# Kernel tuning notes

Measured on AMD Instinct MI355X. Metric: run time of the kernel, lower is better.

Reference implementation:

```python
import jax, jax.numpy as jnp
import numpy as np

C = 512
NUM_HEADS = 8
NUM_GROUPS = 32
EPS = 1e-6


def group_norm(x, gamma, beta):
    # x: [B, C, N]
    b, c, n = x.shape
    xg = x.reshape(b, NUM_GROUPS, (c // NUM_GROUPS) * n)
    mean = xg.mean(axis=-1, keepdims=True)
    var = xg.var(axis=-1, keepdims=True)
    xg = (xg - mean) * jax.lax.rsqrt(var + EPS)
    x = xg.reshape(b, c, n)
    return x * gamma[None, :, None] + beta[None, :, None]


def conv1x1(x, w, bias):
    # pointwise conv: w [out_c, in_c], x [B, C, N]
    return jnp.einsum('oc,bcn->bon', w, x) + bias[None, :, None]


def setup_inputs() -> dict:
    key = jax.random.key(0)
    ks = jax.random.split(key, 11)
    s = 1.0 / np.sqrt(C)
    inp = {
        'x': jax.random.normal(ks[0], (4, C, 2048), dtype=jnp.float32),
        'gn_gamma': jnp.ones((C,), jnp.float32),
        'gn_beta': jnp.zeros((C,), jnp.float32),
        'q_w': jax.random.uniform(ks[1], (C, C), jnp.float32, -s, s),
        'q_b': jax.random.uniform(ks[2], (C,), jnp.float32, -s, s),
        'k_w': jax.random.uniform(ks[3], (C, C), jnp.float32, -s, s),
        'k_b': jax.random.uniform(ks[4], (C,), jnp.float32, -s, s),
        'v_w': jax.random.uniform(ks[5], (C, C), jnp.float32, -s, s),
        'v_b': jax.random.uniform(ks[6], (C,), jnp.float32, -s, s),
        'proj_w': jax.random.uniform(ks[7], (C, C), jnp.float32, -s, s),
        'proj_b': jax.random.uniform(ks[8], (C,), jnp.float32, -s, s),
    }
    return inp


def reference(x, gn_gamma, gn_beta, q_w, q_b, k_w, k_b, v_w, v_b, proj_w, proj_b):
    b, c, n = x.shape
    hc = c // NUM_HEADS
    h_ = group_norm(x, gn_gamma, gn_beta)
    q = conv1x1(h_, q_w, q_b)
    k = conv1x1(h_, k_w, k_b)
    v = conv1x1(h_, v_w, v_b)
    # split heads: [B, H, hc, N]
    q = q.reshape(b, NUM_HEADS, hc, n)
    k = k.reshape(b, NUM_HEADS, hc, n)
    v = v.reshape(b, NUM_HEADS, hc, n)
    # NOTE: scale uses full channel count c, matching the original code
    scale = jnp.asarray(c, x.dtype) ** -0.5
    # scores: [B, H, Nq, Nk]
    w = jnp.einsum('bhcn,bhcm->bhnm', q, k) * scale
    w = jax.nn.softmax(w, axis=-1)
    # out[b,h,c,q] = sum_m v[b,h,c,m] * w[b,h,q,m]
    out = jnp.einsum('bhcm,bhqm->bhcq', v, w)
    out = out.reshape(b, c, n)
    out = conv1x1(out, proj_w, proj_b)
    return x + out
```

## Files before the change

kernel.cpp:

```cpp
#include <hip/hip_runtime.h>
#include <hip/hip_bf16.h>
#include <math.h>

#define C_DIM 512
#define N_DIM 2048
#define B_DIM 4
#define NGRP 32
#define GCH 16
#define NHEAD 8
#define HDIM 64
#define EPSV 1e-6f

using f32x4  = __attribute__((ext_vector_type(4))) float;
using bf16x8 = __attribute__((ext_vector_type(8))) short;

#define GLL16(gp, lp) __builtin_amdgcn_global_load_lds( \
    (const __attribute__((address_space(1))) unsigned int*)(gp), \
    (__attribute__((address_space(3))) unsigned int*)(lp), 16, 0, 0)

#define BFPACK(a, b) __builtin_amdgcn_perm(__float_as_uint(b), __float_as_uint(a), 0x07060302u)

static __device__ __forceinline__ unsigned short f2bf(float f) {
    union { __hip_bfloat16 h; unsigned short u; } cv;
    cv.h = __float2bfloat16(f);
    return cv.u;
}

__global__ __launch_bounds__(256) void gn_stats(const float* __restrict__ x,
                                                float* __restrict__ partial) {
    const int HSZ = GCH * N_DIM / 2;
    int blk = blockIdx.x;
    const float4* x4 = (const float4*)(x + (size_t)blk * HSZ);
    int tid = threadIdx.x;

    float s = 0.f, ss = 0.f;
    #pragma unroll
    for (int it = 0; it < HSZ / 4 / 256; ++it) {
        float4 v = x4[tid + it * 256];
        s  += v.x + v.y + v.z + v.w;
        ss += v.x * v.x + v.y * v.y + v.z * v.z + v.w * v.w;
    }
    __shared__ float rs[256], rss[256];
    rs[tid] = s; rss[tid] = ss;
    __syncthreads();
    for (int off = 128; off > 0; off >>= 1) {
        if (tid < off) { rs[tid] += rs[tid + off]; rss[tid] += rss[tid + off]; }
        __syncthreads();
    }
    if (tid == 0) {
        partial[blk * 2]     = rs[0];
        partial[blk * 2 + 1] = rss[0];
    }
}

__global__ __launch_bounds__(256) void gn_apply_t(const float* __restrict__ x,
                                                  const float* __restrict__ partial,
                                                  const float* __restrict__ gamma,
                                                  const float* __restrict__ beta,
                                                  unsigned short* __restrict__ ht) {
    __shared__ char smem[8192];
    const float GSZI = 1.f / (GCH * N_DIM);
    int n0 = blockIdx.x * 64, c0 = blockIdx.y * 64, b = blockIdx.z;
    int tid = threadIdx.x;
    #pragma unroll
    for (int it = 0; it < 4; ++it) {
        int idx = tid + it * 256;
        int ci = idx >> 4, n4 = (idx & 15) << 2;
        int cg = c0 + ci, grp = cg >> 4;
        int bg = b * NGRP + grp;
        float s  = partial[bg * 4]     + partial[bg * 4 + 2];
        float ss = partial[bg * 4 + 1] + partial[bg * 4 + 3];
        float mean = s * GSZI;
        float var  = ss * GSZI - mean * mean;
        float rstd = rsqrtf(var + EPSV);
        float ga = gamma[cg] * rstd, be = beta[cg] - mean * ga;
        float4 v = *(const float4*)&x[((size_t)b * C_DIM + cg) * N_DIM + n0 + n4];
        float vals[4] = {v.x, v.y, v.z, v.w};
        #pragma unroll
        for (int j = 0; j < 4; ++j) {
            int nl = n4 + j;
            *(unsigned short*)(smem + nl * 128 + ((ci * 2) ^ ((nl & 7) << 4))) =
                f2bf(vals[j] * ga + be);
        }
    }
    __syncthreads();
    #pragma unroll
    for (int i = 0; i < 2; ++i) {
        int idx = tid + i * 256;
        int row = idx >> 3, ch = idx & 7;
        bf16x8 v = *(const bf16x8*)(smem + row * 128 + ((ch * 16) ^ ((row & 7) << 4)));
        *(bf16x8*)&ht[((size_t)(b * N_DIM + n0 + row)) * C_DIM + c0 + ch * 8] = v;
    }
}

__global__ __launch_bounds__(256) void cast4_bf16(const float* __restrict__ s0,
                                                  const float* __restrict__ s1,
                                                  const float* __restrict__ s2,
                                                  const float* __restrict__ s3,
                                                  unsigned short* __restrict__ dst) {
    int which = blockIdx.y;
    const float* src = (which == 0) ? s0 : (which == 1) ? s1 : (which == 2) ? s2 : s3;
    size_t idx = (size_t)blockIdx.x * 256 + threadIdx.x;
    const float4* s4 = (const float4*)src;
    float4 a = s4[idx * 2], b = s4[idx * 2 + 1];
    bf16x8 o;
    o[0] = (short)f2bf(a.x); o[1] = (short)f2bf(a.y);
    o[2] = (short)f2bf(a.z); o[3] = (short)f2bf(a.w);
    o[4] = (short)f2bf(b.x); o[5] = (short)f2bf(b.y);
    o[6] = (short)f2bf(b.z); o[7] = (short)f2bf(b.w);
    *(bf16x8*)&dst[(size_t)which * 262144 + idx * 8] = o;
}

__global__ __launch_bounds__(512) void conv_qkv(const unsigned short* __restrict__ Wall,
                                                const float* __restrict__ q_b,
                                                const float* __restrict__ k_b,
                                                const float* __restrict__ v_b,
                                                const unsigned short* __restrict__ ht,
                                                unsigned short* __restrict__ qt,
                                                unsigned short* __restrict__ kt,
                                                unsigned short* __restrict__ vt,
                                                float escale) {
    __shared__ char smem[40960];

    int bn0 = blockIdx.x * 128;
    int bo  = blockIdx.y * 64;
    int tid = threadIdx.x;
    int L = tid & 63, w = tid >> 6;
    int g = L >> 4, c = L & 15;
    int wr = w >> 2, wc = w & 3;

    f32x4 acc[3][2][2];
    #pragma unroll
    for (int w3 = 0; w3 < 3; ++w3)
        #pragma unroll
        for (int t = 0; t < 2; ++t)
            #pragma unroll
            for (int u = 0; u < 2; ++u) acc[w3][t][u] = f32x4{0.f, 0.f, 0.f, 0.f};

    for (int k0 = 0; k0 < C_DIM; k0 += 64) {
        if (w < 4) {
            #pragma unroll
            for (int i = 0; i < 4; ++i) {
                int j = w * 4 + i;
                int row = j * 8 + (L >> 3);
                int sl = (L & 7) ^ (row & 7);
                GLL16(ht + (size_t)(bn0 + row) * C_DIM + k0 + sl * 8, smem + j * 1024);
            }
        } else {
            #pragma unroll
            for (int i = 0; i < 6; ++i) {
                int j = (w - 4) * 6 + i;
                int w3 = j >> 3, jj = j & 7;
                int row = jj * 8 + (L >> 3);
                int sl = (L & 7) ^ (row & 7);
                GLL16(Wall + (size_t)w3 * 262144 + (size_t)(bo + row) * C_DIM + k0 + sl * 8,
                      smem + 16384 + j * 1024);
            }
        }
        __syncthreads();

        bf16x8 bfr[2][2];
        #pragma unroll
        for (int u = 0; u < 2; ++u) {
            int row = wc * 32 + u * 16 + c;
            #pragma unroll
            for (int ks = 0; ks < 2; ++ks)
                bfr[u][ks] = *(const bf16x8*)(smem + row * 128 +
                                              ((g * 16 + ks * 64) ^ ((row & 7) << 4)));
        }
        #pragma unroll
        for (int w3 = 0; w3 < 3; ++w3) {
            char* As = smem + 16384 + w3 * 8192;
            bf16x8 af[2][2];
            #pragma unroll
            for (int t = 0; t < 2; ++t) {
                int row = wr * 32 + t * 16 + c;
                #pragma unroll
                for (int ks = 0; ks < 2; ++ks)
                    af[t][ks] = *(const bf16x8*)(As + row * 128 +
                                                 ((g * 16 + ks * 64) ^ ((row & 7) << 4)));
            }
            #pragma unroll
            for (int ks = 0; ks < 2; ++ks)
                #pragma unroll
                for (int t = 0; t < 2; ++t)
                    #pragma unroll
                    for (int u = 0; u < 2; ++u)
                        acc[w3][t][u] = __builtin_amdgcn_mfma_f32_16x16x32_bf16(
                            af[t][ks], bfr[u][ks], acc[w3][t][u], 0, 0, 0);
        }
        __syncthreads();
    }

    int b  = bn0 >> 11;
    int nb = bn0 & (N_DIM - 1);
    int hh = bo >> 6;
    int bh = b * NHEAD + hh;

    #pragma unroll
    for (int t = 0; t < 2; ++t)
        #pragma unroll
        for (int r = 0; r < 4; ++r) {
            int m = bo + wr * 32 + t * 16 + g * 4 + r;
            float bi = v_b[m];
            #pragma unroll
            for (int u = 0; u < 2; ++u) {
                int n = nb + wc * 32 + u * 16 + c;
                vt[((size_t)b * C_DIM + m) * N_DIM + n] = f2bf(acc[2][t][u][r] + bi);
            }
        }

    char* Ts = smem;
    #pragma unroll
    for (int pass = 0; pass < 2; ++pass) {
        const float* bias = pass ? k_b : q_b;
        float esc = pass ? 1.0f : escale;
        unsigned short* dst = pass ? kt : qt;
        __syncthreads();
        #pragma unroll
        for (int t = 0; t < 2; ++t)
            #pragma unroll
            for (int r = 0; r < 4; ++r) {
                int ml = wr * 32 + t * 16 + g * 4 + r;
                float bi = bias[bo + ml];
                #pragma unroll
                for (int u = 0; u < 2; ++u) {
                    int nl = wc * 32 + u * 16 + c;
                    *(unsigned short*)(Ts + nl * 128 + ((ml * 2) ^ ((nl & 7) << 4))) =
                        f2bf((acc[pass][t][u][r] + bi) * esc);
                }
            }
        __syncthreads();
        #pragma unroll
        for (int i = 0; i < 2; ++i) {
            int idx = tid + i * 512;
            int row = idx >> 3, ch = idx & 7;
            bf16x8 v = *(const bf16x8*)(Ts + row * 128 + ((ch * 16) ^ ((row & 7) << 4)));
            *(bf16x8*)&dst[((size_t)bh * N_DIM + nb + row) * HDIM + ch * 8] = v;
        }
    }
}

__global__ __launch_bounds__(256) void conv_proj(const unsigned short* __restrict__ Wb,
                                                 const float* __restrict__ bias,
                                                 const unsigned short* __restrict__ Bsrc,
                                                 const float* __restrict__ res,
                                                 float* __restrict__ outf) {
    __shared__ char smem[24576];
    int bn0 = blockIdx.x * 128;
    int bo  = blockIdx.y * 64;
    int tid = threadIdx.x;
    int L = tid & 63, w = tid >> 6;
    int g = L >> 4, c = L & 15;
    int wr = w >> 1, wc = w & 1;

    f32x4 acc[2][4];
    #pragma unroll
    for (int t = 0; t < 2; ++t)
        #pragma unroll
        for (int u = 0; u < 4; ++u) acc[t][u] = f32x4{0.f, 0.f, 0.f, 0.f};

    for (int k0 = 0; k0 < C_DIM; k0 += 64) {
        #pragma unroll
        for (int i = 0; i < 2; ++i) {
            int j = w * 2 + i;
            int ra = j * 8 + (L >> 3);
            int sl = (L & 7) ^ (ra & 7);
            GLL16(Wb + (size_t)(bo + ra) * C_DIM + k0 + sl * 8, smem + j * 1024);
        }
        #pragma unroll
        for (int i = 0; i < 4; ++i) {
            int j = w * 4 + i;
            int rb = j * 8 + (L >> 3);
            int sl = (L & 7) ^ (rb & 7);
            GLL16(Bsrc + (size_t)(bn0 + rb) * C_DIM + k0 + sl * 8, smem + 8192 + j * 1024);
        }
        __syncthreads();

        bf16x8 af[2][2], bfr[4][2];
        #pragma unroll
        for (int t = 0; t < 2; ++t) {
            int row = wr * 32 + t * 16 + c;
            #pragma unroll
            for (int ks = 0; ks < 2; ++ks)
                af[t][ks] = *(const bf16x8*)(smem + row * 128 +
                                             ((g * 16 + ks * 64) ^ ((row & 7) << 4)));
        }
        #pragma unroll
        for (int u = 0; u < 4; ++u) {
            int row = wc * 64 + u * 16 + c;
            #pragma unroll
            for (int ks = 0; ks < 2; ++ks)
                bfr[u][ks] = *(const bf16x8*)(smem + 8192 + row * 128 +
                                              ((g * 16 + ks * 64) ^ ((row & 7) << 4)));
        }
        #pragma unroll
        for (int ks = 0; ks < 2; ++ks)
            #pragma unroll
            for (int t = 0; t < 2; ++t)
                #pragma unroll
                for (int u = 0; u < 4; ++u)
                    acc[t][u] = __builtin_amdgcn_mfma_f32_16x16x32_bf16(
                        af[t][ks], bfr[u][ks], acc[t][u], 0, 0, 0);
        __syncthreads();
    }

    int b  = bn0 >> 11;
    int nb = bn0 & (N_DIM - 1);
    #pragma unroll
    for (int t = 0; t < 2; ++t)
        #pragma unroll
        for (int r = 0; r < 4; ++r) {
            int m = bo + wr * 32 + t * 16 + g * 4 + r;
            float bi = bias[m];
            #pragma unroll
            for (int u = 0; u < 4; ++u) {
                int n = nb + wc * 64 + u * 16 + c;
                size_t off = ((size_t)b * C_DIM + m) * N_DIM + n;
                outf[off] = acc[t][u][r] + bi + res[off];
            }
        }
}

__global__ __launch_bounds__(512, 4) void attn_kernel(const unsigned short* __restrict__ Qt,
                                                      const unsigned short* __restrict__ Kt,
                                                      const unsigned short* __restrict__ Vt,
                                                      unsigned short* __restrict__ at) {
    __shared__ char smem[49152];

    int d = blockIdx.x;
    int xcd = d & 7;
    int slot = d >> 3;
    int bh = xcd + 8 * (slot >> 4);
    int q0 = (slot & 15) * 128;

    int b = bh >> 3, hh = bh & 7;
    int tid = threadIdx.x;
    int L = tid & 63, w = tid >> 6;
    int g = L >> 4, c = L & 15;

    const unsigned short* Qh = Qt + (size_t)bh * N_DIM * HDIM;
    const unsigned short* Kh = Kt + (size_t)bh * N_DIM * HDIM;
    const unsigned short* Vh = Vt + (size_t)bh * HDIM * N_DIM;

    #pragma unroll
    for (int i = 0; i < 2; ++i) {
        int j = w * 2 + i;
        int row = j * 8 + (L >> 3);
        int sl = (L & 7) ^ (row & 7);
        GLL16(Qh + (size_t)(q0 + row) * HDIM + sl * 8, smem + j * 1024);
    }
    int srow = w * 8 + (L >> 3);
    int ssl  = (L & 7) ^ (srow & 7);
    GLL16(Kh + (size_t)srow * HDIM + ssl * 8, smem + 16384 + w * 1024);
    GLL16(Vh + (size_t)srow * N_DIM + ssl * 8, smem + 24576 + w * 1024);
    __syncthreads();

    int csw = (c & 7) << 4;
    char* kb0 = smem + 16384 + c * 128 + ((g * 16) ^ csw);
    char* kb1 = smem + 16384 + c * 128 + ((g * 16 + 64) ^ csw);
    char* pb  = smem + (w * 16 + c) * 128;
    char* pw0 = pb + ((g * 8) ^ csw);
    char* pw1 = pb + ((32 + g * 8) ^ csw);
    char* pw2 = pb + ((64 + g * 8) ^ csw);
    char* pw3 = pb + ((96 + g * 8) ^ csw);
    char* pr0 = pb + ((g * 16) ^ csw);
    char* pr1 = pb + ((64 + g * 16) ^ csw);

    bf16x8 qf[2];
    qf[0] = *(const bf16x8*)pr0;
    qf[1] = *(const bf16x8*)pr1;

    const unsigned short* kgp = Kh + (size_t)(64 + srow) * HDIM + ssl * 8;
    const unsigned short* vgp = Vh + (size_t)srow * N_DIM + 64 + ssl * 8;

    f32x4 oacc[4];
    #pragma unroll
    for (int t = 0; t < 4; ++t) oacc[t] = f32x4{0.f, 0.f, 0.f, 0.f};
    float m_r = -INFINITY, l_part = 0.f;

    auto tile = [&](int BOFF) {
        f32x4 sacc[4];
        #pragma unroll
        for (int t = 0; t < 4; ++t) sacc[t] = f32x4{0.f, 0.f, 0.f, 0.f};
        __builtin_amdgcn_s_setprio(1);
        #pragma unroll
        for (int t = 0; t < 4; ++t) {
            bf16x8 kf0 = *(const bf16x8*)(kb0 + BOFF + t * 2048);
            bf16x8 kf1 = *(const bf16x8*)(kb1 + BOFF + t * 2048);
            sacc[t] = __builtin_amdgcn_mfma_f32_16x16x32_bf16(kf0, qf[0], sacc[t], 0, 0, 0);
            sacc[t] = __builtin_amdgcn_mfma_f32_16x16x32_bf16(kf1, qf[1], sacc[t], 0, 0, 0);
        }
        __builtin_amdgcn_s_setprio(0);

        float t0 = fmaxf(fmaxf(sacc[0][0], sacc[0][1]), sacc[0][2]);
        float t1 = fmaxf(fmaxf(sacc[0][3], sacc[1][0]), sacc[1][1]);
        float t2 = fmaxf(fmaxf(sacc[1][2], sacc[1][3]), sacc[2][0]);
        float t3 = fmaxf(fmaxf(sacc[2][1], sacc[2][2]), sacc[2][3]);
        float t4 = fmaxf(fmaxf(sacc[3][0], sacc[3][1]), sacc[3][2]);
        float mloc = fmaxf(fmaxf(fmaxf(t0, t1), fmaxf(t2, t3)), fmaxf(t4, sacc[3][3]));
        if (!__all(mloc - m_r <= 6.0f)) {
            mloc = fmaxf(mloc, __shfl_xor(mloc, 16));
            mloc = fmaxf(mloc, __shfl_xor(mloc, 32));
            float mn = fmaxf(m_r, mloc);
            float fac = exp2f(m_r - mn);
            m_r = mn;
            l_part *= fac;
            #pragma unroll
            for (int t = 0; t < 4; ++t) oacc[t] = oacc[t] * fac;
        }
        f32x4 m4 = {m_r, m_r, m_r, m_r};
        f32x4 p[4];
        #pragma unroll
        for (int t = 0; t < 4; ++t) {
            f32x4 dd = sacc[t] - m4;
            p[t][0] = exp2f(dd[0]);
            p[t][1] = exp2f(dd[1]);
            p[t][2] = exp2f(dd[2]);
            p[t][3] = exp2f(dd[3]);
        }
        f32x4 racc = (p[0] + p[1]) + (p[2] + p[3]);
        l_part += (racc[0] + racc[1]) + (racc[2] + racc[3]);

        unsigned pk[4][2];
        #pragma unroll
        for (int t = 0; t < 4; ++t) {
            pk[t][0] = BFPACK(p[t][0], p[t][1]);
            pk[t][1] = BFPACK(p[t][2], p[t][3]);
        }

        *(unsigned long long*)pw0 = (unsigned long long)pk[0][0] | ((unsigned long long)pk[0][1] << 32);
        *(unsigned long long*)pw1 = (unsigned long long)pk[1][0] | ((unsigned long long)pk[1][1] << 32);
        *(unsigned long long*)pw2 = (unsigned long long)pk[2][0] | ((unsigned long long)pk[2][1] << 32);
        *(unsigned long long*)pw3 = (unsigned long long)pk[3][0] | ((unsigned long long)pk[3][1] << 32);

        __builtin_amdgcn_s_setprio(1);
        {
            bf16x8 pf0 = *(const bf16x8*)pr0;
            #pragma unroll
            for (int t = 0; t < 4; ++t) {
                bf16x8 vf = *(const bf16x8*)(kb0 + BOFF + 8192 + t * 2048);
                oacc[t] = __builtin_amdgcn_mfma_f32_16x16x32_bf16(vf, pf0, oacc[t], 0, 0, 0);
            }
            bf16x8 pf1 = *(const bf16x8*)pr1;
            #pragma unroll
            for (int t = 0; t < 4; ++t) {
                bf16x8 vf = *(const bf16x8*)(kb1 + BOFF + 8192 + t * 2048);
                oacc[t] = __builtin_amdgcn_mfma_f32_16x16x32_bf16(vf, pf1, oacc[t], 0, 0, 0);
            }
        }
        __builtin_amdgcn_s_setprio(0);
    };

    #define ATTN_BARRIER() do { \
        __builtin_amdgcn_s_barrier(); \
        asm volatile("" ::: "memory"); \
    } while (0)
    #define ATTN_VMCNT2() do { \
        asm volatile("s_waitcnt vmcnt(2)" ::: "memory"); \
        __builtin_amdgcn_sched_barrier(0); \
    } while (0)
    #define ATTN_VMCNT0() do { \
        asm volatile("s_waitcnt vmcnt(0)" ::: "memory"); \
        __builtin_amdgcn_sched_barrier(0); \
    } while (0)

    for (int i = 0; i < 15; ++i) {
        ATTN_BARRIER();
        GLL16(kgp, smem + 32768 + w * 1024);
        GLL16(vgp, smem + 40960 + w * 1024);
        kgp += 64 * HDIM;
        vgp += 64;
        ATTN_VMCNT2();
        tile(0);
        ATTN_BARRIER();
        GLL16(kgp, smem + 16384 + w * 1024);
        GLL16(vgp, smem + 24576 + w * 1024);
        kgp += 64 * HDIM;
        vgp += 64;
        ATTN_VMCNT2();
        tile(16384);
    }
    ATTN_BARRIER();
    GLL16(kgp, smem + 32768 + w * 1024);
    GLL16(vgp, smem + 40960 + w * 1024);
    ATTN_VMCNT2();
    tile(0);
    ATTN_BARRIER();
    ATTN_VMCNT0();
    tile(16384);

    #undef ATTN_BARRIER
    #undef ATTN_VMCNT2
    #undef ATTN_VMCNT0

    float l_r = l_part;
    l_r += __shfl_xor(l_r, 16);
    l_r += __shfl_xor(l_r, 32);
    float oinv = 1.f / l_r;
    {
        unsigned lo, hi;
        lo = BFPACK(oacc[0][0] * oinv, oacc[0][1] * oinv);
        hi = BFPACK(oacc[0][2] * oinv, oacc[0][3] * oinv);
        *(unsigned long long*)pw0 = (unsigned long long)lo | ((unsigned long long)hi << 32);
        lo = BFPACK(oacc[1][0] * oinv, oacc[1][1] * oinv);
        hi = BFPACK(oacc[1][2] * oinv, oacc[1][3] * oinv);
        *(unsigned long long*)pw1 = (unsigned long long)lo | ((unsigned long long)hi << 32);
        lo = BFPACK(oacc[2][0] * oinv, oacc[2][1] * oinv);
        hi = BFPACK(oacc[2][2] * oinv, oacc[2][3] * oinv);
        *(unsigned long long*)pw2 = (unsigned long long)lo | ((unsigned long long)hi << 32);
        lo = BFPACK(oacc[3][0] * oinv, oacc[3][1] * oinv);
        hi = BFPACK(oacc[3][2] * oinv, oacc[3][3] * oinv);
        *(unsigned long long*)pw3 = (unsigned long long)lo | ((unsigned long long)hi << 32);
    }
    char* wbase = smem + w * 2048;
    #pragma unroll
    for (int i = 0; i < 2; ++i) {
        int idx = L + i * 64;
        int row = idx >> 3, ch = idx & 7;
        bf16x8 v = *(const bf16x8*)(wbase + row * 128 + ((ch * 16) ^ ((row & 7) << 4)));
        *(bf16x8*)&at[((size_t)(b * N_DIM + q0 + w * 16 + row)) * C_DIM + hh * HDIM + ch * 8] = v;
    }
}

extern "C" void kernel_launch(void* const* d_in, const int* in_sizes, int n_in,
                              void* d_out, int out_size, void* d_ws, size_t ws_size,
                              hipStream_t stream) {
    (void)in_sizes; (void)n_in; (void)out_size; (void)ws_size;
    const float* x     = (const float*)d_in[0];
    const float* gam   = (const float*)d_in[1];
    const float* bet   = (const float*)d_in[2];
    const float* q_w   = (const float*)d_in[3];
    const float* q_b   = (const float*)d_in[4];
    const float* k_w   = (const float*)d_in[5];
    const float* k_b   = (const float*)d_in[6];
    const float* v_w   = (const float*)d_in[7];
    const float* v_b   = (const float*)d_in[8];
    const float* p_w   = (const float*)d_in[9];
    const float* p_b   = (const float*)d_in[10];
    float* out = (float*)d_out;

    const size_t MB = 1 << 20;
    char* wsb = (char*)d_ws;
    unsigned short* ht  = (unsigned short*)(wsb);
    unsigned short* wqb = (unsigned short*)(wsb + 8 * MB);
    unsigned short* wpb = (unsigned short*)(wsb + 9 * MB + 512 * 1024);
    float*          partial = (float*)(wsb + 10 * MB);
    unsigned short* qt  = (unsigned short*)(wsb + 11 * MB);
    unsigned short* kt  = (unsigned short*)(wsb + 19 * MB);
    unsigned short* vt  = (unsigned short*)(wsb + 27 * MB);
    unsigned short* at  = (unsigned short*)(wsb + 35 * MB);

    gn_stats<<<B_DIM * NGRP * 2, 256, 0, stream>>>(x, partial);
    gn_apply_t<<<dim3(N_DIM / 64, C_DIM / 64, B_DIM), 256, 0, stream>>>(x, partial, gam, bet, ht);

    cast4_bf16<<<dim3(128, 4), 256, 0, stream>>>(q_w, k_w, v_w, p_w, wqb);

    const float escale = 0.044194173824159216f * 1.4426950408889634f;
    conv_qkv<<<dim3(B_DIM * N_DIM / 128, C_DIM / 64), 512, 0, stream>>>(
        wqb, q_b, k_b, v_b, ht, qt, kt, vt, escale);

    attn_kernel<<<512, 512, 0, stream>>>(qt, kt, vt, at);

    conv_proj<<<dim3(B_DIM * N_DIM / 128, C_DIM / 64), 256, 0, stream>>>(wpb, p_b, at, x, out);
}
```

Before: 113.4 us.

## Process two query sub-tiles per wave in attention to reuse K/V fragments

The attention kernel moves from 8 waves with 16 query rows each to 4 waves with 32 query rows each, held as two sub-tiles sharing every K and V fragment read from LDS. This halves LDS reads of K/V per query row and gives each wave more independent MFMAs to interleave. Each thread now issues twice as many async loads per stage, so the waitcnt changes from vmcnt(2) to vmcnt(4). The cost is higher register pressure and fewer waves per block to hide latency, with launch bounds moving from (512,4) to (256,2).

```diff
diff --git a/kernel.cpp b/kernel.cpp
--- a/kernel.cpp
+++ b/kernel.cpp
@@ -322,7 +322,7 @@
         }
 }
 
-__global__ __launch_bounds__(512, 4) void attn_kernel(const unsigned short* __restrict__ Qt,
+__global__ __launch_bounds__(256, 2) void attn_kernel(const unsigned short* __restrict__ Qt,
                                                       const unsigned short* __restrict__ Kt,
                                                       const unsigned short* __restrict__ Vt,
                                                       unsigned short* __restrict__ at) {
@@ -343,110 +343,134 @@
     const unsigned short* Kh = Kt + (size_t)bh * N_DIM * HDIM;
     const unsigned short* Vh = Vt + (size_t)bh * HDIM * N_DIM;
 
-    #pragma unroll
-    for (int i = 0; i < 2; ++i) {
-        int j = w * 2 + i;
+    int ssl = (L & 7) ^ (L >> 3);
+    #pragma unroll
+    for (int i = 0; i < 4; ++i) {
+        int j = w * 4 + i;
         int row = j * 8 + (L >> 3);
-        int sl = (L & 7) ^ (row & 7);
-        GLL16(Qh + (size_t)(q0 + row) * HDIM + sl * 8, smem + j * 1024);
-    }
-    int srow = w * 8 + (L >> 3);
-    int ssl  = (L & 7) ^ (srow & 7);
-    GLL16(Kh + (size_t)srow * HDIM + ssl * 8, smem + 16384 + w * 1024);
-    GLL16(Vh + (size_t)srow * N_DIM + ssl * 8, smem + 24576 + w * 1024);
+        GLL16(Qh + (size_t)(q0 + row) * HDIM + ssl * 8, smem + j * 1024);
+    }
+    int srow = w * 16 + (L >> 3);
+    GLL16(Kh + (size_t)srow * HDIM + ssl * 8,        smem + 16384 + (2 * w) * 1024);
+    GLL16(Kh + (size_t)(srow + 8) * HDIM + ssl * 8,  smem + 16384 + (2 * w + 1) * 1024);
+    GLL16(Vh + (size_t)srow * N_DIM + ssl * 8,       smem + 24576 + (2 * w) * 1024);
+    GLL16(Vh + (size_t)(srow + 8) * N_DIM + ssl * 8, smem + 24576 + (2 * w + 1) * 1024);
     __syncthreads();
 
     int csw = (c & 7) << 4;
     char* kb0 = smem + 16384 + c * 128 + ((g * 16) ^ csw);
     char* kb1 = smem + 16384 + c * 128 + ((g * 16 + 64) ^ csw);
-    char* pb  = smem + (w * 16 + c) * 128;
-    char* pw0 = pb + ((g * 8) ^ csw);
-    char* pw1 = pb + ((32 + g * 8) ^ csw);
-    char* pw2 = pb + ((64 + g * 8) ^ csw);
-    char* pw3 = pb + ((96 + g * 8) ^ csw);
-    char* pr0 = pb + ((g * 16) ^ csw);
-    char* pr1 = pb + ((64 + g * 16) ^ csw);
-
-    bf16x8 qf[2];
-    qf[0] = *(const bf16x8*)pr0;
-    qf[1] = *(const bf16x8*)pr1;
+    char* pb  = smem + (w * 32 + c) * 128;
+    int pwo0 = (g * 8) ^ csw;
+    int pwo1 = (32 + g * 8) ^ csw;
+    int pwo2 = (64 + g * 8) ^ csw;
+    int pwo3 = (96 + g * 8) ^ csw;
+    int pro0 = (g * 16) ^ csw;
+    int pro1 = (64 + g * 16) ^ csw;
+
+    bf16x8 qf[2][2];
+    #pragma unroll
+    for (int s = 0; s < 2; ++s) {
+        qf[s][0] = *(const bf16x8*)(pb + s * 2048 + pro0);
+        qf[s][1] = *(const bf16x8*)(pb + s * 2048 + pro1);
+    }
 
     const unsigned short* kgp = Kh + (size_t)(64 + srow) * HDIM + ssl * 8;
     const unsigned short* vgp = Vh + (size_t)srow * N_DIM + 64 + ssl * 8;
 
-    f32x4 oacc[4];
-    #pragma unroll
-    for (int t = 0; t < 4; ++t) oacc[t] = f32x4{0.f, 0.f, 0.f, 0.f};
-    float m_r = -INFINITY, l_part = 0.f;
+    f32x4 oacc[2][4];
+    #pragma unroll
+    for (int s = 0; s < 2; ++s)
+        #pragma unroll
+        for (int t = 0; t < 4; ++t) oacc[s][t] = f32x4{0.f, 0.f, 0.f, 0.f};
+    float m_r[2] = {-INFINITY, -INFINITY};
+    float l_part[2] = {0.f, 0.f};
 
     auto tile = [&](int BOFF) {
-        f32x4 sacc[4];
-        #pragma unroll
-        for (int t = 0; t < 4; ++t) sacc[t] = f32x4{0.f, 0.f, 0.f, 0.f};
+        f32x4 sacc[2][4];
+        #pragma unroll
+        for (int s = 0; s < 2; ++s)
+            #pragma unroll
+            for (int t = 0; t < 4; ++t) sacc[s][t] = f32x4{0.f, 0.f, 0.f, 0.f};
         __builtin_amdgcn_s_setprio(1);
         #pragma unroll
         for (int t = 0; t < 4; ++t) {
             bf16x8 kf0 = *(const bf16x8*)(kb0 + BOFF + t * 2048);
             bf16x8 kf1 = *(const bf16x8*)(kb1 + BOFF + t * 2048);
-            sacc[t] = __builtin_amdgcn_mfma_f32_16x16x32_bf16(kf0, qf[0], sacc[t], 0, 0, 0);
-            sacc[t] = __builtin_amdgcn_mfma_f32_16x16x32_bf16(kf1, qf[1], sacc[t], 0, 0, 0);
+            sacc[0][t] = __builtin_amdgcn_mfma_f32_16x16x32_bf16(kf0, qf[0][0], sacc[0][t], 0, 0, 0);
+            sacc[0][t] = __builtin_amdgcn_mfma_f32_16x16x32_bf16(kf1, qf[0][1], sacc[0][t], 0, 0, 0);
+            sacc[1][t] = __builtin_amdgcn_mfma_f32_16x16x32_bf16(kf0, qf[1][0], sacc[1][t], 0, 0, 0);
+            sacc[1][t] = __builtin_amdgcn_mfma_f32_16x16x32_bf16(kf1, qf[1][1], sacc[1][t], 0, 0, 0);
         }
         __builtin_amdgcn_s_setprio(0);
 
-        float t0 = fmaxf(fmaxf(sacc[0][0], sacc[0][1]), sacc[0][2]);
-        float t1 = fmaxf(fmaxf(sacc[0][3], sacc[1][0]), sacc[1][1]);
-        float t2 = fmaxf(fmaxf(sacc[1][2], sacc[1][3]), sacc[2][0]);
-        float t3 = fmaxf(fmaxf(sacc[2][1], sacc[2][2]), sacc[2][3]);
-        float t4 = fmaxf(fmaxf(sacc[3][0], sacc[3][1]), sacc[3][2]);
-        float mloc = fmaxf(fmaxf(fmaxf(t0, t1), fmaxf(t2, t3)), fmaxf(t4, sacc[3][3]));
-        if (!__all(mloc - m_r <= 6.0f)) {
-            mloc = fmaxf(mloc, __shfl_xor(mloc, 16));
-            mloc = fmaxf(mloc, __shfl_xor(mloc, 32));
-            float mn = fmaxf(m_r, mloc);
-            float fac = exp2f(m_r - mn);
-            m_r = mn;
-            l_part *= fac;
-            #pragma unroll
-            for (int t = 0; t < 4; ++t) oacc[t] = oacc[t] * fac;
-        }
-        f32x4 m4 = {m_r, m_r, m_r, m_r};
-        f32x4 p[4];
-        #pragma unroll
-        for (int t = 0; t < 4; ++t) {
-            f32x4 dd = sacc[t] - m4;
-            p[t][0] = exp2f(dd[0]);
-            p[t][1] = exp2f(dd[1]);
-            p[t][2] = exp2f(dd[2]);
-            p[t][3] = exp2f(dd[3]);
-        }
-        f32x4 racc = (p[0] + p[1]) + (p[2] + p[3]);
-        l_part += (racc[0] + racc[1]) + (racc[2] + racc[3]);
-
-        unsigned pk[4][2];
-        #pragma unroll
-        for (int t = 0; t < 4; ++t) {
-            pk[t][0] = BFPACK(p[t][0], p[t][1]);
-            pk[t][1] = BFPACK(p[t][2], p[t][3]);
-        }
-
-        *(unsigned long long*)pw0 = (unsigned long long)pk[0][0] | ((unsigned long long)pk[0][1] << 32);
-        *(unsigned long long*)pw1 = (unsigned long long)pk[1][0] | ((unsigned long long)pk[1][1] << 32);
-        *(unsigned long long*)pw2 = (unsigned long long)pk[2][0] | ((unsigned long long)pk[2][1] << 32);
-        *(unsigned long long*)pw3 = (unsigned long long)pk[3][0] | ((unsigned long long)pk[3][1] << 32);
+        float mloc[2];
+        #pragma unroll
+        for (int s = 0; s < 2; ++s) {
+            float t0 = fmaxf(fmaxf(sacc[s][0][0], sacc[s][0][1]), sacc[s][0][2]);
+            float t1 = fmaxf(fmaxf(sacc[s][0][3], sacc[s][1][0]), sacc[s][1][1]);
+            float t2 = fmaxf(fmaxf(sacc[s][1][2], sacc[s][1][3]), sacc[s][2][0]);
+            float t3 = fmaxf(fmaxf(sacc[s][2][1], sacc[s][2][2]), sacc[s][2][3]);
+            float t4 = fmaxf(fmaxf(sacc[s][3][0], sacc[s][3][1]), sacc[s][3][2]);
+            mloc[s] = fmaxf(fmaxf(fmaxf(t0, t1), fmaxf(t2, t3)), fmaxf(t4, sacc[s][3][3]));
+        }
+        float growth = fmaxf(mloc[0] - m_r[0], mloc[1] - m_r[1]);
+        if (!__all(growth <= 6.0f)) {
+            #pragma unroll
+            for (int s = 0; s < 2; ++s) {
+                float ms = mloc[s];
+                ms = fmaxf(ms, __shfl_xor(ms, 16));
+                ms = fmaxf(ms, __shfl_xor(ms, 32));
+                float mn = fmaxf(m_r[s], ms);
+                float fac = exp2f(m_r[s] - mn);
+                m_r[s] = mn;
+                l_part[s] *= fac;
+                #pragma unroll
+                for (int t = 0; t < 4; ++t) oacc[s][t] = oacc[s][t] * fac;
+            }
+        }
+        unsigned pk[2][4][2];
+        #pragma unroll
+        for (int s = 0; s < 2; ++s) {
+            f32x4 m4 = {m_r[s], m_r[s], m_r[s], m_r[s]};
+            f32x4 p[4];
+            #pragma unroll
+            for (int t = 0; t < 4; ++t) {
+                f32x4 dd = sacc[s][t] - m4;
+                p[t][0] = exp2f(dd[0]);
+                p[t][1] = exp2f(dd[1]);
+                p[t][2] = exp2f(dd[2]);
+                p[t][3] = exp2f(dd[3]);
+            }
+            f32x4 racc = (p[0] + p[1]) + (p[2] + p[3]);
+            l_part[s] += (racc[0] + racc[1]) + (racc[2] + racc[3]);
+            #pragma unroll
+            for (int t = 0; t < 4; ++t) {
+                pk[s][t][0] = BFPACK(p[t][0], p[t][1]);
+                pk[s][t][1] = BFPACK(p[t][2], p[t][3]);
+            }
+        }
+
+        #pragma unroll
+        for (int s = 0; s < 2; ++s) {
+            char* sb = pb + s * 2048;
+            *(unsigned long long*)(sb + pwo0) = (unsigned long long)pk[s][0][0] | ((unsigned long long)pk[s][0][1] << 32);
+            *(unsigned long long*)(sb + pwo1) = (unsigned long long)pk[s][1][0] | ((unsigned long long)pk[s][1][1] << 32);
+            *(unsigned long long*)(sb + pwo2) = (unsigned long long)pk[s][2][0] | ((unsigned long long)pk[s][2][1] << 32);
+            *(unsigned long long*)(sb + pwo3) = (unsigned long long)pk[s][3][0] | ((unsigned long long)pk[s][3][1] << 32);
+        }
 
         __builtin_amdgcn_s_setprio(1);
-        {
-            bf16x8 pf0 = *(const bf16x8*)pr0;
+        #pragma unroll
+        for (int ks = 0; ks < 2; ++ks) {
+            char* kbase = (ks == 0 ? kb0 : kb1) + BOFF + 8192;
+            bf16x8 pf0 = *(const bf16x8*)(pb + (ks ? pro1 : pro0));
+            bf16x8 pf1 = *(const bf16x8*)(pb + 2048 + (ks ? pro1 : pro0));
             #pragma unroll
             for (int t = 0; t < 4; ++t) {
-                bf16x8 vf = *(const bf16x8*)(kb0 + BOFF + 8192 + t * 2048);
-                oacc[t] = __builtin_amdgcn_mfma_f32_16x16x32_bf16(vf, pf0, oacc[t], 0, 0, 0);
-            }
-            bf16x8 pf1 = *(const bf16x8*)pr1;
-            #pragma unroll
-            for (int t = 0; t < 4; ++t) {
-                bf16x8 vf = *(const bf16x8*)(kb1 + BOFF + 8192 + t * 2048);
-                oacc[t] = __builtin_amdgcn_mfma_f32_16x16x32_bf16(vf, pf1, oacc[t], 0, 0, 0);
+                bf16x8 vf = *(const bf16x8*)(kbase + t * 2048);
+                oacc[0][t] = __builtin_amdgcn_mfma_f32_16x16x32_bf16(vf, pf0, oacc[0][t], 0, 0, 0);
+                oacc[1][t] = __builtin_amdgcn_mfma_f32_16x16x32_bf16(vf, pf1, oacc[1][t], 0, 0, 0);
             }
         }
         __builtin_amdgcn_s_setprio(0);
@@ -456,8 +480,8 @@
         __builtin_amdgcn_s_barrier(); \
         asm volatile("" ::: "memory"); \
     } while (0)
-    #define ATTN_VMCNT2() do { \
-        asm volatile("s_waitcnt vmcnt(2)" ::: "memory"); \
+    #define ATTN_VMCNT4() do { \
+        asm volatile("s_waitcnt vmcnt(4)" ::: "memory"); \
         __builtin_amdgcn_sched_barrier(0); \
     } while (0)
     #define ATTN_VMCNT0() do { \
@@ -467,59 +491,67 @@
 
     for (int i = 0; i < 15; ++i) {
         ATTN_BARRIER();
-        GLL16(kgp, smem + 32768 + w * 1024);
-        GLL16(vgp, smem + 40960 + w * 1024);
+        GLL16(kgp,              smem + 32768 + (2 * w) * 1024);
+        GLL16(kgp + 8 * HDIM,   smem + 32768 + (2 * w + 1) * 1024);
+        GLL16(vgp,              smem + 40960 + (2 * w) * 1024);
+        GLL16(vgp + 8 * N_DIM,  smem + 40960 + (2 * w + 1) * 1024);
         kgp += 64 * HDIM;
         vgp += 64;
-        ATTN_VMCNT2();
+        ATTN_VMCNT4();
         tile(0);
         ATTN_BARRIER();
-        GLL16(kgp, smem + 16384 + w * 1024);
-        GLL16(vgp, smem + 24576 + w * 1024);
+        GLL16(kgp,              smem + 16384 + (2 * w) * 1024);
+        GLL16(kgp + 8 * HDIM,   smem + 16384 + (2 * w + 1) * 1024);
+        GLL16(vgp,              smem + 24576 + (2 * w) * 1024);
+        GLL16(vgp + 8 * N_DIM,  smem + 24576 + (2 * w + 1) * 1024);
         kgp += 64 * HDIM;
         vgp += 64;
-        ATTN_VMCNT2();
+        ATTN_VMCNT4();
         tile(16384);
     }
     ATTN_BARRIER();
-    GLL16(kgp, smem + 32768 + w * 1024);
-    GLL16(vgp, smem + 40960 + w * 1024);
-    ATTN_VMCNT2();
+    GLL16(kgp,              smem + 32768 + (2 * w) * 1024);
+    GLL16(kgp + 8 * HDIM,   smem + 32768 + (2 * w + 1) * 1024);
+    GLL16(vgp,              smem + 40960 + (2 * w) * 1024);
+    GLL16(vgp + 8 * N_DIM,  smem + 40960 + (2 * w + 1) * 1024);
+    ATTN_VMCNT4();
     tile(0);
     ATTN_BARRIER();
     ATTN_VMCNT0();
     tile(16384);
 
     #undef ATTN_BARRIER
-    #undef ATTN_VMCNT2
+    #undef ATTN_VMCNT4
     #undef ATTN_VMCNT0
 
-    float l_r = l_part;
-    l_r += __shfl_xor(l_r, 16);
-    l_r += __shfl_xor(l_r, 32);
-    float oinv = 1.f / l_r;
-    {
+    #pragma unroll
+    for (int s = 0; s < 2; ++s) {
+        float l_r = l_part[s];
+        l_r += __shfl_xor(l_r, 16);
+        l_r += __shfl_xor(l_r, 32);
+        float oinv = 1.f / l_r;
+        char* sb = pb + s * 2048;
         unsigned lo, hi;
-        lo = BFPACK(oacc[0][0] * oinv, oacc[0][1] * oinv);
-        hi = BFPACK(oacc[0][2] * oinv, oacc[0][3] * oinv);
-        *(unsigned long long*)pw0 = (unsigned long long)lo | ((unsigned long long)hi << 32);
-        lo = BFPACK(oacc[1][0] * oinv, oacc[1][1] * oinv);
-        hi = BFPACK(oacc[1][2] * oinv, oacc[1][3] * oinv);
-        *(unsigned long long*)pw1 = (unsigned long long)lo | ((unsigned long long)hi << 32);
-        lo = BFPACK(oacc[2][0] * oinv, oacc[2][1] * oinv);
-        hi = BFPACK(oacc[2][2] * oinv, oacc[2][3] * oinv);
-        *(unsigned long long*)pw2 = (unsigned long long)lo | ((unsigned long long)hi << 32);
-        lo = BFPACK(oacc[3][0] * oinv, oacc[3][1] * oinv);
-        hi = BFPACK(oacc[3][2] * oinv, oacc[3][3] * oinv);
-        *(unsigned long long*)pw3 = (unsigned long long)lo | ((unsigned long long)hi << 32);
-    }
-    char* wbase = smem + w * 2048;
-    #pragma unroll
-    for (int i = 0; i < 2; ++i) {
+        lo = BFPACK(oacc[s][0][0] * oinv, oacc[s][0][1] * oinv);
+        hi = BFPACK(oacc[s][0][2] * oinv, oacc[s][0][3] * oinv);
+        *(unsigned long long*)(sb + pwo0) = (unsigned long long)lo | ((unsigned long long)hi << 32);
+        lo = BFPACK(oacc[s][1][0] * oinv, oacc[s][1][1] * oinv);
+        hi = BFPACK(oacc[s][1][2] * oinv, oacc[s][1][3] * oinv);
+        *(unsigned long long*)(sb + pwo1) = (unsigned long long)lo | ((unsigned long long)hi << 32);
+        lo = BFPACK(oacc[s][2][0] * oinv, oacc[s][2][1] * oinv);
+        hi = BFPACK(oacc[s][2][2] * oinv, oacc[s][2][3] * oinv);
+        *(unsigned long long*)(sb + pwo2) = (unsigned long long)lo | ((unsigned long long)hi << 32);
+        lo = BFPACK(oacc[s][3][0] * oinv, oacc[s][3][1] * oinv);
+        hi = BFPACK(oacc[s][3][2] * oinv, oacc[s][3][3] * oinv);
+        *(unsigned long long*)(sb + pwo3) = (unsigned long long)lo | ((unsigned long long)hi << 32);
+    }
+    char* wbase = smem + w * 4096;
+    #pragma unroll
+    for (int i = 0; i < 4; ++i) {
         int idx = L + i * 64;
         int row = idx >> 3, ch = idx & 7;
         bf16x8 v = *(const bf16x8*)(wbase + row * 128 + ((ch * 16) ^ ((row & 7) << 4)));
-        *(bf16x8*)&at[((size_t)(b * N_DIM + q0 + w * 16 + row)) * C_DIM + hh * HDIM + ch * 8] = v;
+        *(bf16x8*)&at[((size_t)(b * N_DIM + q0 + w * 32 + row)) * C_DIM + hh * HDIM + ch * 8] = v;
     }
 }
 
@@ -560,7 +592,7 @@
     conv_qkv<<<dim3(B_DIM * N_DIM / 128, C_DIM / 64), 512, 0, stream>>>(
         wqb, q_b, k_b, v_b, ht, qt, kt, vt, escale);
 
-    attn_kernel<<<512, 512, 0, stream>>>(qt, kt, vt, at);
+    attn_kernel<<<512, 256, 0, stream>>>(qt, kt, vt, at);
 
     conv_proj<<<dim3(B_DIM * N_DIM / 128, C_DIM / 64), 256, 0, stream>>>(wpb, p_b, at, x, out);
 }
```

New measurement: 121.2 us. +6.9%, slower.
